# Kernel tuning notes

Hardware: AMD Instinct MI355X
Metric: run time of the kernel (lower is better)

## Reference

```python
import jax, jax.numpy as jnp
import numpy as np

DIM = 1024
NUM_HEADS = 16
HEAD_DIM = DIM // NUM_HEADS
B, S = 2, 2048


def setup_inputs() -> dict:
    key = jax.random.key(0)
    ks = jax.random.split(key, 12)
    sc = 1.0 / np.sqrt(DIM)
    inp = {
        'x': jax.random.normal(ks[0], (B, S, DIM), dtype=jnp.float32),
        'Wq': jax.random.normal(ks[1], (DIM, DIM), dtype=jnp.float32) * sc,
        'bq': jnp.zeros((DIM,), dtype=jnp.float32),
        'Wk': jax.random.normal(ks[2], (DIM, DIM), dtype=jnp.float32) * sc,
        'bk': jnp.zeros((DIM,), dtype=jnp.float32),
        'Wv': jax.random.normal(ks[3], (DIM, DIM), dtype=jnp.float32) * sc,
        'bv': jnp.zeros((DIM,), dtype=jnp.float32),
        'Wg1': jax.random.normal(ks[4], (DIM, DIM // 2), dtype=jnp.float32) * sc,
        'bg1': jnp.zeros((DIM // 2,), dtype=jnp.float32),
        'Wg2': jax.random.normal(ks[5], (DIM // 2, NUM_HEADS), dtype=jnp.float32) * (1.0 / np.sqrt(DIM // 2)),
        'bg2': jnp.zeros((NUM_HEADS,), dtype=jnp.float32),
        'Wo': jax.random.normal(ks[6], (DIM, DIM), dtype=jnp.float32) * sc,
        'bo': jnp.zeros((DIM,), dtype=jnp.float32),
    }
    return inp


def reference(x, Wq, bq, Wk, bk, Wv, bv, Wg1, bg1, Wg2, bg2, Wo, bo):
    b, s, dim = x.shape
    h, d = NUM_HEADS, HEAD_DIM
    # QKV projections -> (b, h, s, d)
    q = (x @ Wq + bq).reshape(b, s, h, d).transpose(0, 2, 1, 3)
    k = (x @ Wk + bk).reshape(b, s, h, d).transpose(0, 2, 1, 3)
    v = (x @ Wv + bv).reshape(b, s, h, d).transpose(0, 2, 1, 3)
    # raw attention scores (b, h, q, k)
    scores = jnp.einsum('bhqd,bhkd->bhqk', q, k) / np.sqrt(d)
    # superposition gate: per-(batch, token) softmax over heads -> (b, s, h)
    gate = jax.nn.softmax(jnp.tanh(x @ Wg1 + bg1) @ Wg2 + bg2, axis=-1)
    gate = gate.transpose(0, 2, 1)[..., None]  # (b, h, s, 1) -- per-query scale
    scores = scores * gate
    probs = jax.nn.softmax(scores, axis=-1)
    # dropout is identity at inference
    attended = jnp.einsum('bhqk,bhkd->bhqd', probs, v)
    attended = attended.transpose(0, 2, 1, 3).reshape(b, s, dim)
    return attended @ Wo + bo
```

## Files before the change

kernel.cpp:

```cpp
#include <hip/hip_runtime.h>
#include <math.h>

#define DIM    1024
#define NHEADS 16
#define HDIM   64
#define BATCH  2
#define SEQ    2048
#define TOK    (BATCH * SEQ)

typedef unsigned short ushort;
typedef __attribute__((ext_vector_type(8))) short  short8;
typedef __attribute__((ext_vector_type(4))) float  f32x4;
typedef __attribute__((ext_vector_type(4))) unsigned short us4;

__device__ __forceinline__ ushort f2bf(float f) {
    unsigned u = __float_as_uint(f);
    u += 0x7fffu + ((u >> 16) & 1u);
    return (ushort)(u >> 16);
}
__device__ __forceinline__ float bf2f(ushort h) {
    return __uint_as_float(((unsigned)h) << 16);
}
__device__ __forceinline__ unsigned cvt_pk_bf16(float a, float b) {
    unsigned r;
    asm("v_cvt_pk_bf16_f32 %0, %1, %2" : "=v"(r) : "v"(a), "v"(b));
    return r;
}

__device__ __forceinline__ void gload16(const void* g, void* lds) {
    __builtin_amdgcn_global_load_lds(
        (const __attribute__((address_space(1))) unsigned int*)g,
        (__attribute__((address_space(3))) unsigned int*)lds, 16, 0, 0);
}

__global__ __launch_bounds__(256) void split_hl(
    const float* __restrict__ in, ushort* __restrict__ hi, ushort* __restrict__ lo)
{
    const int i = blockIdx.x * 256 + threadIdx.x;
    float4 v = ((const float4*)in)[i];
    us4 h, l;
    h.x = f2bf(v.x); l.x = f2bf(v.x - bf2f(h.x));
    h.y = f2bf(v.y); l.y = f2bf(v.y - bf2f(h.y));
    h.z = f2bf(v.z); l.z = f2bf(v.z - bf2f(h.z));
    h.w = f2bf(v.w); l.w = f2bf(v.w - bf2f(h.w));
    ((us4*)hi)[i] = h;
    ((us4*)lo)[i] = l;
}

__device__ __forceinline__ void tsplit_body(
    const float* __restrict__ in, ushort* __restrict__ hiT, ushort* __restrict__ loT,
    int K, int N, int k0, int n0)
{
    __shared__ float t[32][33];
    const int x = threadIdx.x & 31, y = threadIdx.x >> 5;
#pragma unroll
    for (int r = 0; r < 4; ++r)
        t[y + r * 8][x] = in[(size_t)(k0 + y + r * 8) * N + n0 + x];
    __syncthreads();
#pragma unroll
    for (int r = 0; r < 4; ++r) {
        const int row = y + r * 8;
        const float v = t[x][row];
        const ushort h = f2bf(v);
        const size_t o = (size_t)(n0 + row) * K + k0 + x;
        hiT[o] = h;
        loT[o] = f2bf(v - bf2f(h));
    }
}

__global__ __launch_bounds__(256) void wsplitT(
    const float* __restrict__ W0, const float* __restrict__ W1,
    const float* __restrict__ W2, const float* __restrict__ W3,
    const float* __restrict__ Wg1,
    ushort* __restrict__ hiT, ushort* __restrict__ loT,
    ushort* __restrict__ g1hiT, ushort* __restrict__ g1loT)
{
    const int z = blockIdx.z;
    if (z < 4) {
        const float* in = (z == 0) ? W0 : (z == 1) ? W1 : (z == 2) ? W2 : W3;
        tsplit_body(in, hiT + (size_t)z * DIM * DIM, loT + (size_t)z * DIM * DIM,
                    DIM, DIM, blockIdx.y * 32, blockIdx.x * 32);
    } else {
        if (blockIdx.x >= 16) return;
        tsplit_body(Wg1, g1hiT, g1loT, DIM, 512, blockIdx.y * 32, blockIdx.x * 32);
    }
}

template<int MREP>
__device__ __forceinline__ void mgemm_core(
    const ushort* __restrict__ Ahi, const ushort* __restrict__ Alo,
    const ushort* __restrict__ BThi, const ushort* __restrict__ BTlo,
    const float* __restrict__ bias, int act, int store, int npass,
    float* __restrict__ Cf, ushort* __restrict__ Ch, ushort* __restrict__ Cl,
    int ldc, int row0, int col0, ushort* ldsA, ushort* ldsB)
{
    const int tid  = threadIdx.x;
    const int lane = tid & 63;
    const int wid  = tid >> 6;
    const int wr   = wid >> 1;
    const int wc   = wid & 1;
    const int l15  = lane & 15;
    const int l4   = lane >> 4;

    f32x4 acc[MREP][4];
#pragma unroll
    for (int m = 0; m < MREP; ++m)
#pragma unroll
        for (int n = 0; n < 4; ++n) acc[m][n] = (f32x4){0.f, 0.f, 0.f, 0.f};

    const int trow = wid * 8 + (lane >> 3);
    const int swz  = ((lane & 7) ^ (lane >> 3)) * 8;

    for (int ph = 0; ph < npass; ++ph) {
        const ushort* Ap = (ph == 1) ? Alo : Ahi;
        const ushort* Bp = (ph == 2) ? BTlo : BThi;
        const ushort* Asrc = Ap + (size_t)(row0 + trow) * 1024 + swz;
        const ushort* Bsrc = Bp + (size_t)(col0 + trow) * 1024 + swz;

        for (int k0 = 0; k0 < 1024; k0 += 64) {
            __syncthreads();
#pragma unroll
            for (int r = 0; r < MREP; ++r)
                gload16(Asrc + (size_t)r * 32 * 1024 + k0, &ldsA[(wid * 8 + r * 32) * 64]);
#pragma unroll
            for (int r = 0; r < 4; ++r)
                gload16(Bsrc + (size_t)r * 32 * 1024 + k0, &ldsB[(wid * 8 + r * 32) * 64]);
            __syncthreads();

#pragma unroll
            for (int s = 0; s < 2; ++s) {
                short8 a[MREP], b[4];
#pragma unroll
                for (int m = 0; m < MREP; ++m) {
                    const int row = wr * (MREP * 16) + m * 16 + l15;
                    a[m] = *(const short8*)&ldsA[row * 64 + (((s * 4 + l4) ^ (row & 7)) * 8)];
                }
#pragma unroll
                for (int n = 0; n < 4; ++n) {
                    const int row = wc * 64 + n * 16 + l15;
                    b[n] = *(const short8*)&ldsB[row * 64 + (((s * 4 + l4) ^ (row & 7)) * 8)];
                }
#pragma unroll
                for (int m = 0; m < MREP; ++m)
#pragma unroll
                    for (int n = 0; n < 4; ++n)
                        acc[m][n] = __builtin_amdgcn_mfma_f32_16x16x32_bf16(
                            a[m], b[n], acc[m][n], 0, 0, 0);
            }
        }
    }

#pragma unroll
    for (int m = 0; m < MREP; ++m)
#pragma unroll
        for (int n = 0; n < 4; ++n) {
            const int c = col0 + wc * 64 + n * 16 + l15;
            const float bc = bias[c];
            f32x4 v = acc[m][n];
            if (store == 4) {
                const int r0 = row0 + wr * (MREP * 16) + m * 16 + l4 * 4;
                const int bb = r0 >> 11, s0 = r0 & (SEQ - 1);
                const int hh = c >> 6,  d = c & (HDIM - 1);
                us4 pk;
#pragma unroll
                for (int rg = 0; rg < 4; ++rg) pk[rg] = f2bf(v[rg] + bc);
                *(us4*)&Ch[(((size_t)bb * NHEADS + hh) * HDIM + d) * SEQ + s0] = pk;
                continue;
            }
#pragma unroll
            for (int rg = 0; rg < 4; ++rg) {
                const int r = row0 + wr * (MREP * 16) + m * 16 + l4 * 4 + rg;
                float o = v[rg] + bc;
                if (act == 1) o = tanhf(o);
                if (store == 0) {
                    Cf[(size_t)r * ldc + c] = o;
                } else if (store == 1) {
                    const int bb = r >> 11, s = r & (SEQ - 1);
                    const int hh = c >> 6,  d = c & (HDIM - 1);
                    Cf[(((size_t)bb * NHEADS + hh) * SEQ + s) * HDIM + d] = o;
                } else {
                    const int bb = r >> 11, s = r & (SEQ - 1);
                    const int hh = c >> 6,  d = c & (HDIM - 1);
                    const size_t off = (((size_t)bb * NHEADS + hh) * SEQ + s) * HDIM + d;
                    const ushort hb = f2bf(o);
                    Ch[off] = hb;
                    if (store == 2) Cl[off] = f2bf(o - bf2f(hb));
                }
            }
        }
}

__global__ __launch_bounds__(256) void mgemm_fused(
    const ushort* __restrict__ xhi, const ushort* __restrict__ xlo,
    const ushort* __restrict__ WThi, const ushort* __restrict__ WTlo,
    const ushort* __restrict__ Wg1Thi, const ushort* __restrict__ Wg1Tlo,
    const float* __restrict__ bq, const float* __restrict__ bk,
    const float* __restrict__ bv, const float* __restrict__ bg1,
    ushort* __restrict__ qhB, ushort* __restrict__ qlB,
    ushort* __restrict__ khB, ushort* __restrict__ klB,
    ushort* __restrict__ vTB, float* __restrict__ Hb)
{
    __shared__ ushort ldsA[128 * 64];
    __shared__ ushort ldsB[128 * 64];

    const int y = blockIdx.y;
    const ushort *Bh, *Bl;
    const float* bias;
    int act = 0, store, npass, ldc = DIM, col0;
    float* Cf = nullptr;
    ushort *Ch = nullptr, *Cl = nullptr;

    if (y < 24) {
        const int sel = y >> 3;
        col0 = (y & 7) * 128;
        const size_t off = (size_t)sel * DIM * DIM;
        Bh = WThi + off; Bl = WTlo + off;
        if (sel == 0)      { bias = bq; store = 2; npass = 3; Ch = qhB; Cl = qlB; }
        else if (sel == 1) { bias = bk; store = 2; npass = 3; Ch = khB; Cl = klB; }
        else               { bias = bv; store = 4; npass = 1; Ch = vTB; }
    } else {
        col0 = (y - 24) * 128;
        Bh = Wg1Thi; Bl = Wg1Tlo; bias = bg1;
        act = 1; store = 0; npass = 2; Cf = Hb; ldc = 512;
    }
    mgemm_core<4>(xhi, xlo, Bh, Bl, bias, act, store, npass, Cf, Ch, Cl, ldc,
                  blockIdx.x * 128, col0, ldsA, ldsB);
}

__global__ __launch_bounds__(256) void mgemm_out(
    const ushort* __restrict__ Ahi, const ushort* __restrict__ Alo,
    const ushort* __restrict__ BThi, const ushort* __restrict__ BTlo,
    const float* __restrict__ bias, float* __restrict__ Cf)
{
    __shared__ ushort ldsA[64 * 64];
    __shared__ ushort ldsB[128 * 64];
    mgemm_core<2>(Ahi, Alo, BThi, BTlo, bias, 0, 0, 2, Cf, nullptr, nullptr, DIM,
                  blockIdx.x * 64, blockIdx.y * 128, ldsA, ldsB);
}

__global__ __launch_bounds__(256) void gate2_kernel(
    const float* __restrict__ H, const float* __restrict__ Wg2,
    const float* __restrict__ bg2, float* __restrict__ gate)
{
    const int wave = threadIdx.x >> 6;
    const int lane = threadIdx.x & 63;
    const int t    = blockIdx.x * 4 + wave;
    const int hh   = lane >> 2;
    const int p    = lane & 3;

    const float* Hrow = H + (size_t)t * 512;
    float s = 0.f;
    const int k0 = p * 128;
#pragma unroll 8
    for (int kk = 0; kk < 128; kk++)
        s = __builtin_fmaf(Hrow[k0 + kk], Wg2[(k0 + kk) * NHEADS + hh], s);
    s += __shfl_xor(s, 1);
    s += __shfl_xor(s, 2);
    s += bg2[hh];

    float mx = s;
    mx = fmaxf(mx, __shfl_xor(mx, 4));
    mx = fmaxf(mx, __shfl_xor(mx, 8));
    mx = fmaxf(mx, __shfl_xor(mx, 16));
    mx = fmaxf(mx, __shfl_xor(mx, 32));
    const float e = __expf(s - mx);
    float den = e;
    den += __shfl_xor(den, 4);
    den += __shfl_xor(den, 8);
    den += __shfl_xor(den, 16);
    den += __shfl_xor(den, 32);
    if (p == 0) gate[(size_t)t * NHEADS + hh] = e / den;
}

__global__ __launch_bounds__(256, 2) void flash_mfma(
    const ushort* __restrict__ qhi, const ushort* __restrict__ qlo,
    const ushort* __restrict__ khi, const ushort* __restrict__ klo,
    const ushort* __restrict__ vT,
    const float* __restrict__ gate,
    ushort* __restrict__ att_hi, ushort* __restrict__ att_lo)
{
    __shared__ ushort lds[32768];

    const int tid  = threadIdx.x;
    const int lane = tid & 63;
    const int wid  = tid >> 6;
    const int l15  = lane & 15;
    const int l4   = lane >> 4;
    const int qt   = blockIdx.x;
    const int bh   = blockIdx.y;
    const int b    = bh >> 4, h = bh & 15;

    ushort* Pwv = lds + 24576 + wid * 2048;

    short8 qhf[2][2], qlf[2][2];
#pragma unroll
    for (int n = 0; n < 2; n++) {
        const int qrow = qt * 128 + wid * 32 + n * 16 + l15;
        const float g = gate[(size_t)(b * SEQ + qrow) * NHEADS + h] * 0.125f;
        const size_t qoff = ((size_t)bh * SEQ + qrow) * HDIM;
#pragma unroll
        for (int kc = 0; kc < 2; kc++) {
            const int d0 = kc * 32 + l4 * 8;
            short8 h8 = *(const short8*)&qhi[qoff + d0];
            short8 l8 = *(const short8*)&qlo[qoff + d0];
            short8 hh, ll;
#pragma unroll
            for (int j = 0; j < 8; j++) {
                const float t = (bf2f((ushort)h8[j]) + bf2f((ushort)l8[j])) * g;
                const ushort hb = f2bf(t);
                hh[j] = (short)hb;
                ll[j] = (short)f2bf(t - bf2f(hb));
            }
            qhf[n][kc] = hh;
            qlf[n][kc] = ll;
        }
    }

    const ushort* Ksrc_h = khi + (size_t)bh * SEQ * HDIM;
    const ushort* Ksrc_l = klo + (size_t)bh * SEQ * HDIM;
    const ushort* Vsrc   = vT  + (size_t)bh * HDIM * SEQ;

    float m_[2] = {-INFINITY, -INFINITY};
    float l_[2] = {0.f, 0.f};
    f32x4 O[2][4];
#pragma unroll
    for (int mq = 0; mq < 2; mq++)
#pragma unroll
        for (int nd = 0; nd < 4; nd++) O[mq][nd] = (f32x4){0.f, 0.f, 0.f, 0.f};

    auto STAGE = [&](int bufOff, int kt) {
#pragma unroll
        for (int p = 0; p < 2; p++) {
            const int r   = wid * 16 + p * 8 + (lane >> 3);
            const int cs  = ((lane & 7) ^ (r & 7)) * 8;
            ushort* dst = lds + bufOff + (wid * 16 + p * 8) * 64 + lane * 8;
            gload16(Ksrc_h + (size_t)(kt * 64 + r) * HDIM + cs, dst);
            gload16(Ksrc_l + (size_t)(kt * 64 + r) * HDIM + cs, dst + 4096);
            gload16(Vsrc + (size_t)r * SEQ + kt * 64 + cs, dst + 8192);
        }
    };

    auto TILE = [&](int kt, int curOff, bool notLast) {
        if (notLast) {
            STAGE(curOff ^ 12288, kt + 1);
            asm volatile("s_waitcnt vmcnt(6)" ::: "memory");
        } else {
            asm volatile("s_waitcnt vmcnt(0)" ::: "memory");
        }
        __builtin_amdgcn_s_barrier();
        __builtin_amdgcn_sched_barrier(0);

        const ushort* Khi = lds + curOff;
        const ushort* Klo = Khi + 4096;
        const ushort* Vt  = Khi + 8192;

        f32x4 ST[4][2];
#pragma unroll
        for (int mt = 0; mt < 4; mt++)
#pragma unroll
            for (int n = 0; n < 2; n++) ST[mt][n] = (f32x4){0.f, 0.f, 0.f, 0.f};

#pragma unroll
        for (int kc = 0; kc < 2; kc++) {
            short8 ka[4];
#pragma unroll
            for (int mt = 0; mt < 4; mt++) {
                const int row = mt * 16 + l15;
                ka[mt] = *(const short8*)&Khi[row * 64 + (((kc * 4 + l4) ^ (row & 7)) * 8)];
            }
#pragma unroll
            for (int mt = 0; mt < 4; mt++)
#pragma unroll
                for (int n = 0; n < 2; n++)
                    ST[mt][n] = __builtin_amdgcn_mfma_f32_16x16x32_bf16(
                        ka[mt], qhf[n][kc], ST[mt][n], 0, 0, 0);
#pragma unroll
            for (int mt = 0; mt < 4; mt++)
#pragma unroll
                for (int n = 0; n < 2; n++)
                    ST[mt][n] = __builtin_amdgcn_mfma_f32_16x16x32_bf16(
                        ka[mt], qlf[n][kc], ST[mt][n], 0, 0, 0);
        }
#pragma unroll
        for (int kc = 0; kc < 2; kc++) {
            short8 ka[4];
#pragma unroll
            for (int mt = 0; mt < 4; mt++) {
                const int row = mt * 16 + l15;
                ka[mt] = *(const short8*)&Klo[row * 64 + (((kc * 4 + l4) ^ (row & 7)) * 8)];
            }
#pragma unroll
            for (int mt = 0; mt < 4; mt++)
#pragma unroll
                for (int n = 0; n < 2; n++)
                    ST[mt][n] = __builtin_amdgcn_mfma_f32_16x16x32_bf16(
                        ka[mt], qhf[n][kc], ST[mt][n], 0, 0, 0);
        }

        float scn[2];
        bool resc[2];
#pragma unroll
        for (int n = 0; n < 2; n++) {
            float rm = fmaxf(fmaxf(ST[0][n][0], ST[0][n][1]), fmaxf(ST[0][n][2], ST[0][n][3]));
#pragma unroll
            for (int mt = 1; mt < 4; mt++)
                rm = fmaxf(rm, fmaxf(fmaxf(ST[mt][n][0], ST[mt][n][1]),
                                     fmaxf(ST[mt][n][2], ST[mt][n][3])));
            rm = fmaxf(rm, __shfl_xor(rm, 16));
            rm = fmaxf(rm, __shfl_xor(rm, 32));

            resc[n] = !__all(rm <= m_[n] + 8.0f);
            float mn;
            if (resc[n]) {
                mn = fmaxf(m_[n], rm);
                scn[n] = __expf(m_[n] - mn);
                m_[n] = mn;
            } else {
                mn = m_[n];
                scn[n] = 1.0f;
            }

            float ps = 0.f;
#pragma unroll
            for (int mt = 0; mt < 4; mt++)
#pragma unroll
                for (int rg = 0; rg < 4; rg++) {
                    const float e = __expf(ST[mt][n][rg] - mn);
                    ST[mt][n][rg] = e;
                    ps += e;
                }
            ps += __shfl_xor(ps, 16);
            ps += __shfl_xor(ps, 32);
            l_[n] = l_[n] * scn[n] + ps;

            const int qq = n * 16 + l15;
#pragma unroll
            for (int mt = 0; mt < 4; mt++) {
                const unsigned lo32 = cvt_pk_bf16(ST[mt][n][0], ST[mt][n][1]);
                const unsigned hi32 = cvt_pk_bf16(ST[mt][n][2], ST[mt][n][3]);
                const unsigned long long pk = (unsigned long long)lo32 |
                                              ((unsigned long long)hi32 << 32);
                const int slot = (mt * 2 + (l4 >> 1)) ^ (qq & 7);
                *(unsigned long long*)&Pwv[qq * 64 + slot * 8 + (l4 & 1) * 4] = pk;
            }
        }

        if (resc[0] | resc[1]) {
#pragma unroll
            for (int mq = 0; mq < 2; mq++)
#pragma unroll
                for (int rg = 0; rg < 4; rg++) {
                    const float s = __shfl(scn[mq], l4 * 4 + rg);
#pragma unroll
                    for (int nd = 0; nd < 4; nd++) O[mq][nd][rg] *= s;
                }
        }

        asm volatile("s_waitcnt lgkmcnt(0)" ::: "memory");
        __builtin_amdgcn_sched_barrier(0);

#pragma unroll
        for (int kc2 = 0; kc2 < 2; kc2++) {
            short8 ap[2];
#pragma unroll
            for (int mq = 0; mq < 2; mq++) {
                const int qq = mq * 16 + l15;
                ap[mq] = *(const short8*)&Pwv[qq * 64 + (((kc2 * 4 + l4) ^ (qq & 7)) * 8)];
            }
#pragma unroll
            for (int nd = 0; nd < 4; nd++) {
                const int dd = nd * 16 + l15;
                const short8 bv = *(const short8*)&Vt[dd * 64 + (((kc2 * 4 + l4) ^ (dd & 7)) * 8)];
#pragma unroll
                for (int mq = 0; mq < 2; mq++)
                    O[mq][nd] = __builtin_amdgcn_mfma_f32_16x16x32_bf16(
                        ap[mq], bv, O[mq][nd], 0, 0, 0);
            }
        }
        __builtin_amdgcn_s_barrier();
    };

    STAGE(0, 0);
    for (int kt2 = 0; kt2 < SEQ / 64; kt2 += 2) {
        TILE(kt2,     0,     true);
        TILE(kt2 + 1, 12288, kt2 + 1 < SEQ / 64 - 1);
    }

#pragma unroll
    for (int mq = 0; mq < 2; mq++)
#pragma unroll
        for (int rg = 0; rg < 4; rg++) {
            const float linv = 1.f / __shfl(l_[mq], l4 * 4 + rg);
            const int s = qt * 128 + wid * 32 + mq * 16 + l4 * 4 + rg;
#pragma unroll
            for (int nd = 0; nd < 4; nd++) {
                const float o = O[mq][nd][rg] * linv;
                const ushort hb = f2bf(o);
                const size_t off = (size_t)(b * SEQ + s) * DIM + h * HDIM + nd * 16 + l15;
                att_hi[off] = hb;
                att_lo[off] = f2bf(o - bf2f(hb));
            }
        }
}

extern "C" void kernel_launch(void* const* d_in, const int* in_sizes, int n_in,
                              void* d_out, int out_size, void* d_ws, size_t ws_size,
                              hipStream_t stream)
{
    const float* x   = (const float*)d_in[0];
    const float* Wq  = (const float*)d_in[1];
    const float* bq  = (const float*)d_in[2];
    const float* Wk  = (const float*)d_in[3];
    const float* bk  = (const float*)d_in[4];
    const float* Wv  = (const float*)d_in[5];
    const float* bv  = (const float*)d_in[6];
    const float* Wg1 = (const float*)d_in[7];
    const float* bg1 = (const float*)d_in[8];
    const float* Wg2 = (const float*)d_in[9];
    const float* bg2 = (const float*)d_in[10];
    const float* Wo  = (const float*)d_in[11];
    const float* bo  = (const float*)d_in[12];
    float* out = (float*)d_out;

    char* p = (char*)d_ws;
    ushort* qhB   = (ushort*)p;  p += (size_t)TOK * DIM * 2;
    ushort* qlB   = (ushort*)p;  p += (size_t)TOK * DIM * 2;
    ushort* khB   = (ushort*)p;  p += (size_t)TOK * DIM * 2;
    ushort* klB   = (ushort*)p;  p += (size_t)TOK * DIM * 2;
    ushort* vTB   = (ushort*)p;  p += (size_t)TOK * DIM * 2;
    float*  Hb    = (float*)p;   p += (size_t)TOK * 512 * 4;
    float*  gateb = (float*)p;   p += (size_t)TOK * NHEADS * 4;
    ushort* xhi   = (ushort*)p;  p += (size_t)TOK * DIM * 2;
    ushort* xlo   = (ushort*)p;  p += (size_t)TOK * DIM * 2;
    ushort* atth  = (ushort*)p;  p += (size_t)TOK * DIM * 2;
    ushort* attl  = (ushort*)p;  p += (size_t)TOK * DIM * 2;
    ushort* WThi  = (ushort*)p;  p += (size_t)4 * DIM * DIM * 2;
    ushort* WTlo  = (ushort*)p;  p += (size_t)4 * DIM * DIM * 2;
    ushort* Wg1Thi= (ushort*)p;  p += (size_t)512 * DIM * 2;
    ushort* Wg1Tlo= (ushort*)p;  p += (size_t)512 * DIM * 2;

    split_hl<<<TOK * DIM / 4 / 256, 256, 0, stream>>>(x, xhi, xlo);

    wsplitT<<<dim3(32, 32, 5), 256, 0, stream>>>(
        Wq, Wk, Wv, Wo, Wg1, WThi, WTlo, Wg1Thi, Wg1Tlo);

    mgemm_fused<<<dim3(32, 28), 256, 0, stream>>>(
        xhi, xlo, WThi, WTlo, Wg1Thi, Wg1Tlo,
        bq, bk, bv, bg1, qhB, qlB, khB, klB, vTB, Hb);

    gate2_kernel<<<dim3(TOK / 4), 256, 0, stream>>>(Hb, Wg2, bg2, gateb);

    flash_mfma<<<dim3(SEQ / 128, BATCH * NHEADS), 256, 0, stream>>>(
        qhB, qlB, khB, klB, vTB, gateb, atth, attl);

    mgemm_out<<<dim3(64, 8), 256, 0, stream>>>(
        atth, attl, WThi + (size_t)3 * DIM * DIM, WTlo + (size_t)3 * DIM * DIM,
        bo, out);
}
```

Baseline: 331.6 us.

## Drop K low-part split and restructure flash kernel to 8 waves of 16 rows

K is now stored only as bf16 (high part), with a 2-pass store in the projection GEMM, so the QK^T product uses Qhi*K + Qlo*K instead of three MFMA passes, and the Klo loads and buffer go away. The flash kernel moves from 4 waves holding 32 query rows each to 8 waves of 16 rows, using 512 threads and smaller LDS staging, to cut per-wave registers and raise occupancy. This trades away some score precision (K rounding error) and reduces K-tile reuse per wave in exchange for less memory traffic and fewer MFMAs.

```diff
diff --git a/kernel.cpp b/kernel.cpp
--- a/kernel.cpp
+++ b/kernel.cpp
@@ -197,7 +197,7 @@
     const float* __restrict__ bq, const float* __restrict__ bk,
     const float* __restrict__ bv, const float* __restrict__ bg1,
     ushort* __restrict__ qhB, ushort* __restrict__ qlB,
-    ushort* __restrict__ khB, ushort* __restrict__ klB,
+    ushort* __restrict__ khB,
     ushort* __restrict__ vTB, float* __restrict__ Hb)
 {
     __shared__ ushort ldsA[128 * 64];
@@ -216,7 +216,7 @@
         const size_t off = (size_t)sel * DIM * DIM;
         Bh = WThi + off; Bl = WTlo + off;
         if (sel == 0)      { bias = bq; store = 2; npass = 3; Ch = qhB; Cl = qlB; }
-        else if (sel == 1) { bias = bk; store = 2; npass = 3; Ch = khB; Cl = klB; }
+        else if (sel == 1) { bias = bk; store = 3; npass = 2; Ch = khB; }
         else               { bias = bv; store = 4; npass = 1; Ch = vTB; }
     } else {
         col0 = (y - 24) * 128;
@@ -272,14 +272,13 @@
     if (p == 0) gate[(size_t)t * NHEADS + hh] = e / den;
 }
 
-__global__ __launch_bounds__(256, 2) void flash_mfma(
+__global__ __launch_bounds__(512, 4) void flash_mfma(
     const ushort* __restrict__ qhi, const ushort* __restrict__ qlo,
-    const ushort* __restrict__ khi, const ushort* __restrict__ klo,
-    const ushort* __restrict__ vT,
+    const ushort* __restrict__ khi, const ushort* __restrict__ vT,
     const float* __restrict__ gate,
     ushort* __restrict__ att_hi, ushort* __restrict__ att_lo)
 {
-    __shared__ ushort lds[32768];
+    __shared__ ushort lds[24576];
 
     const int tid  = threadIdx.x;
     const int lane = tid & 63;
@@ -290,12 +289,11 @@
     const int bh   = blockIdx.y;
     const int b    = bh >> 4, h = bh & 15;
 
-    ushort* Pwv = lds + 24576 + wid * 2048;
-
-    short8 qhf[2][2], qlf[2][2];
-#pragma unroll
-    for (int n = 0; n < 2; n++) {
-        const int qrow = qt * 128 + wid * 32 + n * 16 + l15;
+    ushort* Pwv = lds + 16384 + wid * 1024;
+
+    short8 qhf[2], qlf[2];
+    {
+        const int qrow = qt * 128 + wid * 16 + l15;
         const float g = gate[(size_t)(b * SEQ + qrow) * NHEADS + h] * 0.125f;
         const size_t qoff = ((size_t)bh * SEQ + qrow) * HDIM;
 #pragma unroll
@@ -311,39 +309,32 @@
                 hh[j] = (short)hb;
                 ll[j] = (short)f2bf(t - bf2f(hb));
             }
-            qhf[n][kc] = hh;
-            qlf[n][kc] = ll;
-        }
-    }
-
-    const ushort* Ksrc_h = khi + (size_t)bh * SEQ * HDIM;
-    const ushort* Ksrc_l = klo + (size_t)bh * SEQ * HDIM;
-    const ushort* Vsrc   = vT  + (size_t)bh * HDIM * SEQ;
-
-    float m_[2] = {-INFINITY, -INFINITY};
-    float l_[2] = {0.f, 0.f};
-    f32x4 O[2][4];
-#pragma unroll
-    for (int mq = 0; mq < 2; mq++)
-#pragma unroll
-        for (int nd = 0; nd < 4; nd++) O[mq][nd] = (f32x4){0.f, 0.f, 0.f, 0.f};
-
+            qhf[kc] = hh;
+            qlf[kc] = ll;
+        }
+    }
+
+    const ushort* Ksrc = khi + (size_t)bh * SEQ * HDIM;
+    const ushort* Vsrc = vT  + (size_t)bh * HDIM * SEQ;
+
+    float m_ = -INFINITY;
+    float l_ = 0.f;
+    f32x4 O[4];
+#pragma unroll
+    for (int nd = 0; nd < 4; nd++) O[nd] = (f32x4){0.f, 0.f, 0.f, 0.f};
+
+    const int srow = wid * 8 + (lane >> 3);
+    const int scs  = ((lane & 7) ^ (srow & 7)) * 8;
     auto STAGE = [&](int bufOff, int kt) {
-#pragma unroll
-        for (int p = 0; p < 2; p++) {
-            const int r   = wid * 16 + p * 8 + (lane >> 3);
-            const int cs  = ((lane & 7) ^ (r & 7)) * 8;
-            ushort* dst = lds + bufOff + (wid * 16 + p * 8) * 64 + lane * 8;
-            gload16(Ksrc_h + (size_t)(kt * 64 + r) * HDIM + cs, dst);
-            gload16(Ksrc_l + (size_t)(kt * 64 + r) * HDIM + cs, dst + 4096);
-            gload16(Vsrc + (size_t)r * SEQ + kt * 64 + cs, dst + 8192);
-        }
+        ushort* dst = lds + bufOff + wid * 512 + lane * 8;
+        gload16(Ksrc + (size_t)(kt * 64 + srow) * HDIM + scs, dst);
+        gload16(Vsrc + (size_t)srow * SEQ + kt * 64 + scs, dst + 4096);
     };
 
     auto TILE = [&](int kt, int curOff, bool notLast) {
         if (notLast) {
-            STAGE(curOff ^ 12288, kt + 1);
-            asm volatile("s_waitcnt vmcnt(6)" ::: "memory");
+            STAGE(curOff ^ 8192, kt + 1);
+            asm volatile("s_waitcnt vmcnt(2)" ::: "memory");
         } else {
             asm volatile("s_waitcnt vmcnt(0)" ::: "memory");
         }
@@ -351,14 +342,11 @@
         __builtin_amdgcn_sched_barrier(0);
 
         const ushort* Khi = lds + curOff;
-        const ushort* Klo = Khi + 4096;
-        const ushort* Vt  = Khi + 8192;
-
-        f32x4 ST[4][2];
-#pragma unroll
-        for (int mt = 0; mt < 4; mt++)
-#pragma unroll
-            for (int n = 0; n < 2; n++) ST[mt][n] = (f32x4){0.f, 0.f, 0.f, 0.f};
+        const ushort* Vt  = Khi + 4096;
+
+        f32x4 ST[4];
+#pragma unroll
+        for (int mt = 0; mt < 4; mt++) ST[mt] = (f32x4){0.f, 0.f, 0.f, 0.f};
 
 #pragma unroll
         for (int kc = 0; kc < 2; kc++) {
@@ -370,90 +358,64 @@
             }
 #pragma unroll
             for (int mt = 0; mt < 4; mt++)
-#pragma unroll
-                for (int n = 0; n < 2; n++)
-                    ST[mt][n] = __builtin_amdgcn_mfma_f32_16x16x32_bf16(
-                        ka[mt], qhf[n][kc], ST[mt][n], 0, 0, 0);
+                ST[mt] = __builtin_amdgcn_mfma_f32_16x16x32_bf16(
+                    ka[mt], qhf[kc], ST[mt], 0, 0, 0);
 #pragma unroll
             for (int mt = 0; mt < 4; mt++)
-#pragma unroll
-                for (int n = 0; n < 2; n++)
-                    ST[mt][n] = __builtin_amdgcn_mfma_f32_16x16x32_bf16(
-                        ka[mt], qlf[n][kc], ST[mt][n], 0, 0, 0);
-        }
-#pragma unroll
-        for (int kc = 0; kc < 2; kc++) {
-            short8 ka[4];
-#pragma unroll
-            for (int mt = 0; mt < 4; mt++) {
-                const int row = mt * 16 + l15;
-                ka[mt] = *(const short8*)&Klo[row * 64 + (((kc * 4 + l4) ^ (row & 7)) * 8)];
-            }
-#pragma unroll
-            for (int mt = 0; mt < 4; mt++)
-#pragma unroll
-                for (int n = 0; n < 2; n++)
-                    ST[mt][n] = __builtin_amdgcn_mfma_f32_16x16x32_bf16(
-                        ka[mt], qhf[n][kc], ST[mt][n], 0, 0, 0);
-        }
-
-        float scn[2];
-        bool resc[2];
-#pragma unroll
-        for (int n = 0; n < 2; n++) {
-            float rm = fmaxf(fmaxf(ST[0][n][0], ST[0][n][1]), fmaxf(ST[0][n][2], ST[0][n][3]));
-#pragma unroll
-            for (int mt = 1; mt < 4; mt++)
-                rm = fmaxf(rm, fmaxf(fmaxf(ST[mt][n][0], ST[mt][n][1]),
-                                     fmaxf(ST[mt][n][2], ST[mt][n][3])));
-            rm = fmaxf(rm, __shfl_xor(rm, 16));
-            rm = fmaxf(rm, __shfl_xor(rm, 32));
-
-            resc[n] = !__all(rm <= m_[n] + 8.0f);
-            float mn;
-            if (resc[n]) {
-                mn = fmaxf(m_[n], rm);
-                scn[n] = __expf(m_[n] - mn);
-                m_[n] = mn;
-            } else {
-                mn = m_[n];
-                scn[n] = 1.0f;
-            }
-
-            float ps = 0.f;
-#pragma unroll
-            for (int mt = 0; mt < 4; mt++)
-#pragma unroll
-                for (int rg = 0; rg < 4; rg++) {
-                    const float e = __expf(ST[mt][n][rg] - mn);
-                    ST[mt][n][rg] = e;
-                    ps += e;
-                }
-            ps += __shfl_xor(ps, 16);
-            ps += __shfl_xor(ps, 32);
-            l_[n] = l_[n] * scn[n] + ps;
-
-            const int qq = n * 16 + l15;
-#pragma unroll
-            for (int mt = 0; mt < 4; mt++) {
-                const unsigned lo32 = cvt_pk_bf16(ST[mt][n][0], ST[mt][n][1]);
-                const unsigned hi32 = cvt_pk_bf16(ST[mt][n][2], ST[mt][n][3]);
-                const unsigned long long pk = (unsigned long long)lo32 |
-                                              ((unsigned long long)hi32 << 32);
-                const int slot = (mt * 2 + (l4 >> 1)) ^ (qq & 7);
-                *(unsigned long long*)&Pwv[qq * 64 + slot * 8 + (l4 & 1) * 4] = pk;
-            }
-        }
-
-        if (resc[0] | resc[1]) {
-#pragma unroll
-            for (int mq = 0; mq < 2; mq++)
-#pragma unroll
-                for (int rg = 0; rg < 4; rg++) {
-                    const float s = __shfl(scn[mq], l4 * 4 + rg);
-#pragma unroll
-                    for (int nd = 0; nd < 4; nd++) O[mq][nd][rg] *= s;
-                }
+                ST[mt] = __builtin_amdgcn_mfma_f32_16x16x32_bf16(
+                    ka[mt], qlf[kc], ST[mt], 0, 0, 0);
+        }
+
+        float rm = fmaxf(fmaxf(ST[0][0], ST[0][1]), fmaxf(ST[0][2], ST[0][3]));
+#pragma unroll
+        for (int mt = 1; mt < 4; mt++)
+            rm = fmaxf(rm, fmaxf(fmaxf(ST[mt][0], ST[mt][1]),
+                                 fmaxf(ST[mt][2], ST[mt][3])));
+        rm = fmaxf(rm, __shfl_xor(rm, 16));
+        rm = fmaxf(rm, __shfl_xor(rm, 32));
+
+        const bool resc = !__all(rm <= m_ + 8.0f);
+        float mn, scn;
+        if (resc) {
+            mn = fmaxf(m_, rm);
+            scn = __expf(m_ - mn);
+            m_ = mn;
+        } else {
+            mn = m_;
+            scn = 1.0f;
+        }
+
+        float ps = 0.f;
+#pragma unroll
+        for (int mt = 0; mt < 4; mt++)
+#pragma unroll
+            for (int rg = 0; rg < 4; rg++) {
+                const float e = __expf(ST[mt][rg] - mn);
+                ST[mt][rg] = e;
+                ps += e;
+            }
+        ps += __shfl_xor(ps, 16);
+        ps += __shfl_xor(ps, 32);
+        l_ = l_ * scn + ps;
+
+        const int qq = l15;
+#pragma unroll
+        for (int mt = 0; mt < 4; mt++) {
+            const unsigned lo32 = cvt_pk_bf16(ST[mt][0], ST[mt][1]);
+            const unsigned hi32 = cvt_pk_bf16(ST[mt][2], ST[mt][3]);
+            const unsigned long long pk = (unsigned long long)lo32 |
+                                          ((unsigned long long)hi32 << 32);
+            const int slot = (mt * 2 + (l4 >> 1)) ^ qq;
+            *(unsigned long long*)&Pwv[qq * 64 + (slot & 7) * 8 + (l4 & 1) * 4] = pk;
+        }
+
+        if (resc) {
+#pragma unroll
+            for (int rg = 0; rg < 4; rg++) {
+                const float s = __shfl(scn, l4 * 4 + rg);
+#pragma unroll
+                for (int nd = 0; nd < 4; nd++) O[nd][rg] *= s;
+            }
         }
 
         asm volatile("s_waitcnt lgkmcnt(0)" ::: "memory");
@@ -461,20 +423,12 @@
 
 #pragma unroll
         for (int kc2 = 0; kc2 < 2; kc2++) {
-            short8 ap[2];
-#pragma unroll
-            for (int mq = 0; mq < 2; mq++) {
-                const int qq = mq * 16 + l15;
-                ap[mq] = *(const short8*)&Pwv[qq * 64 + (((kc2 * 4 + l4) ^ (qq & 7)) * 8)];
-            }
+            const short8 ap = *(const short8*)&Pwv[qq * 64 + (((kc2 * 4 + l4) ^ qq) & 7) * 8];
 #pragma unroll
             for (int nd = 0; nd < 4; nd++) {
                 const int dd = nd * 16 + l15;
                 const short8 bv = *(const short8*)&Vt[dd * 64 + (((kc2 * 4 + l4) ^ (dd & 7)) * 8)];
-#pragma unroll
-                for (int mq = 0; mq < 2; mq++)
-                    O[mq][nd] = __builtin_amdgcn_mfma_f32_16x16x32_bf16(
-                        ap[mq], bv, O[mq][nd], 0, 0, 0);
+                O[nd] = __builtin_amdgcn_mfma_f32_16x16x32_bf16(ap, bv, O[nd], 0, 0, 0);
             }
         }
         __builtin_amdgcn_s_barrier();
@@ -482,25 +436,23 @@
 
     STAGE(0, 0);
     for (int kt2 = 0; kt2 < SEQ / 64; kt2 += 2) {
-        TILE(kt2,     0,     true);
-        TILE(kt2 + 1, 12288, kt2 + 1 < SEQ / 64 - 1);
-    }
-
-#pragma unroll
-    for (int mq = 0; mq < 2; mq++)
-#pragma unroll
-        for (int rg = 0; rg < 4; rg++) {
-            const float linv = 1.f / __shfl(l_[mq], l4 * 4 + rg);
-            const int s = qt * 128 + wid * 32 + mq * 16 + l4 * 4 + rg;
-#pragma unroll
-            for (int nd = 0; nd < 4; nd++) {
-                const float o = O[mq][nd][rg] * linv;
-                const ushort hb = f2bf(o);
-                const size_t off = (size_t)(b * SEQ + s) * DIM + h * HDIM + nd * 16 + l15;
-                att_hi[off] = hb;
-                att_lo[off] = f2bf(o - bf2f(hb));
-            }
-        }
+        TILE(kt2,     0,    true);
+        TILE(kt2 + 1, 8192, kt2 + 1 < SEQ / 64 - 1);
+    }
+
+#pragma unroll
+    for (int rg = 0; rg < 4; rg++) {
+        const float linv = 1.f / __shfl(l_, l4 * 4 + rg);
+        const int s = qt * 128 + wid * 16 + l4 * 4 + rg;
+#pragma unroll
+        for (int nd = 0; nd < 4; nd++) {
+            const float o = O[nd][rg] * linv;
+            const ushort hb = f2bf(o);
+            const size_t off = (size_t)(b * SEQ + s) * DIM + h * HDIM + nd * 16 + l15;
+            att_hi[off] = hb;
+            att_lo[off] = f2bf(o - bf2f(hb));
+        }
+    }
 }
 
 extern "C" void kernel_launch(void* const* d_in, const int* in_sizes, int n_in,
@@ -526,7 +478,6 @@
     ushort* qhB   = (ushort*)p;  p += (size_t)TOK * DIM * 2;
     ushort* qlB   = (ushort*)p;  p += (size_t)TOK * DIM * 2;
     ushort* khB   = (ushort*)p;  p += (size_t)TOK * DIM * 2;
-    ushort* klB   = (ushort*)p;  p += (size_t)TOK * DIM * 2;
     ushort* vTB   = (ushort*)p;  p += (size_t)TOK * DIM * 2;
     float*  Hb    = (float*)p;   p += (size_t)TOK * 512 * 4;
     float*  gateb = (float*)p;   p += (size_t)TOK * NHEADS * 4;
@@ -546,12 +497,12 @@
 
     mgemm_fused<<<dim3(32, 28), 256, 0, stream>>>(
         xhi, xlo, WThi, WTlo, Wg1Thi, Wg1Tlo,
-        bq, bk, bv, bg1, qhB, qlB, khB, klB, vTB, Hb);
+        bq, bk, bv, bg1, qhB, qlB, khB, vTB, Hb);
 
     gate2_kernel<<<dim3(TOK / 4), 256, 0, stream>>>(Hb, Wg2, bg2, gateb);
 
-    flash_mfma<<<dim3(SEQ / 128, BATCH * NHEADS), 256, 0, stream>>>(
-        qhB, qlB, khB, klB, vTB, gateb, atth, attl);
+    flash_mfma<<<dim3(SEQ / 128, BATCH * NHEADS), 512, 0, stream>>>(
+        qhB, qlB, khB, vTB, gateb, atth, attl);
 
     mgemm_out<<<dim3(64, 8), 256, 0, stream>>>(
         atth, attl, WThi + (size_t)3 * DIM * DIM, WTlo + (size_t)3 * DIM * DIM,
```

After: 313.4 us. 5.5% less time.
